# Kernel optimization log

Hardware: AMD Instinct MI355X
Metric: run time of the kernel (lower is better)

The kernel has to match this reference:

```python
import jax, jax.numpy as jnp
import numpy as np

N, D, E, OUT = 10000, 15, 320, 30
H_INOUT = 5  # n_heads for in/out attention layers


def mha(q, k, v, wqkv, bqkv, wo, bo, nheads):
    # q,k,v: [B, L, E]; torch.nn.MultiheadAttention math (unbatched per node)
    B, L, Ed = q.shape
    hd = Ed // nheads
    wq, wk, wv = jnp.split(wqkv, 3, axis=0)
    bq, bk, bv = jnp.split(bqkv, 3)
    q2 = (q @ wq.T + bq).reshape(B, L, nheads, hd)
    k2 = (k @ wk.T + bk).reshape(B, -1, nheads, hd)
    v2 = (v @ wv.T + bv).reshape(B, -1, nheads, hd)
    scores = jnp.einsum('blhd,bmhd->bhlm', q2, k2) * (hd ** -0.5)
    a = jax.nn.softmax(scores, axis=-1)
    o = jnp.einsum('bhlm,bmhd->blhd', a, v2).reshape(B, L, Ed)
    return o @ wo.T + bo


def attn_layer(seq, Wq, Wk, Wv, wqkv, bqkv, wo, bo, nheads):
    # AttentionLayer: custom Q/K/V projections then MultiheadAttention
    return mha(seq @ Wq, seq @ Wk, seq @ Wv, wqkv, bqkv, wo, bo, nheads)


def setup_inputs() -> dict:
    key = jax.random.key(0)
    ks = jax.random.split(key, 24)
    s = 0.05  # scale params small for numerically stable softmax
    inp = {
        'X': jax.random.normal(ks[0], (N, E), jnp.float32),
        'in_idx': jax.random.randint(ks[1], (N, D), 0, N),
        'out_idx': jax.random.randint(ks[2], (N, D), 0, N),
        'in_Wq': jax.random.uniform(ks[3], (E, E)) * s,
        'in_Wk': jax.random.uniform(ks[4], (E, E)) * s,
        'in_Wv': jax.random.uniform(ks[5], (E, E)) * s,
        'in_qkv_w': jax.random.normal(ks[6], (3 * E, E)) * s,
        'in_qkv_b': jax.random.normal(ks[7], (3 * E,)) * s,
        'in_o_w': jax.random.normal(ks[8], (E, E)) * s,
        'in_o_b': jax.random.normal(ks[9], (E,)) * s,
        'out_Wq': jax.random.uniform(ks[10], (E, E)) * s,
        'out_Wk': jax.random.uniform(ks[11], (E, E)) * s,
        'out_Wv': jax.random.uniform(ks[12], (E, E)) * s,
        'out_qkv_w': jax.random.normal(ks[13], (3 * E, E)) * s,
        'out_qkv_b': jax.random.normal(ks[14], (3 * E,)) * s,
        'out_o_w': jax.random.normal(ks[15], (E, E)) * s,
        'out_o_b': jax.random.normal(ks[16], (E,)) * s,
        'fin_qkv_w': jax.random.normal(ks[17], (3 * E, E)) * s,
        'fin_qkv_b': jax.random.normal(ks[18], (3 * E,)) * s,
        'fin_o_w': jax.random.normal(ks[19], (E, E)) * s,
        'fin_o_b': jax.random.normal(ks[20], (E,)) * s,
        'W': jax.random.uniform(ks[21], (E, OUT)) * s,
    }
    return inp


def reference(X, in_idx, out_idx, in_Wq, in_Wk, in_Wv, in_qkv_w, in_qkv_b,
              in_o_w, in_o_b, out_Wq, out_Wk, out_Wv, out_qkv_w, out_qkv_b,
              out_o_w, out_o_b, fin_qkv_w, fin_qkv_b, fin_o_w, fin_o_b, W):
    # per-node sequence: [self ; neighbors] -> [N, D+1, E]
    seq_in = jnp.concatenate([X[:, None, :], X[in_idx]], axis=1)
    seq_out = jnp.concatenate([X[:, None, :], X[out_idx]], axis=1)
    a_in = attn_layer(seq_in, in_Wq, in_Wk, in_Wv, in_qkv_w, in_qkv_b,
                      in_o_w, in_o_b, H_INOUT)
    a_out = attn_layer(seq_out, out_Wq, out_Wk, out_Wv, out_qkv_w, out_qkv_b,
                       out_o_w, out_o_b, H_INOUT)
    att = jnp.concatenate([a_in, a_out], axis=1)  # [N, 2(D+1), E]
    fin = mha(att, att, att, fin_qkv_w, fin_qkv_b, fin_o_w, fin_o_b, 1)
    # first token of final attention per node -> project -> ELU
    return jax.nn.elu(fin[:, 0, :] @ W)
```

## Files before the change

### kernel.cpp

```cpp
#include <hip/hip_runtime.h>
#include <hip/hip_bf16.h>

typedef __hip_bfloat16 bf16;
typedef __bf16 nbf;
typedef nbf bf16x8 __attribute__((ext_vector_type(8)));
typedef float f32x4 __attribute__((ext_vector_type(4)));

#define NNODE 10000
#define DDEG  15
#define EE    320
#define LL    16
#define NH    5
#define HD    64
#define OUTD  30
#define PCOLS 1920
#define KF    642
#define TST   644

__global__ void detect_dtype_kernel(const unsigned int* __restrict__ X, int* __restrict__ flag)
{
    __shared__ int cnt;
    if (threadIdx.x == 0) cnt = 0;
    __syncthreads();
    int local = 0;
    for (int i = threadIdx.x; i < 1024; i += 256) {
        unsigned int lo = X[i] & 0xFFFFu;
        int e = (int)((lo >> 7) & 0xFFu);
        if (e >= 100 && e <= 140) local++;
    }
    atomicAdd(&cnt, local);
    __syncthreads();
    if (threadIdx.x == 0) *flag = (cnt > 512) ? 1 : 0;
}

__global__ void convert_bf_kernel(const void* __restrict__ src, nbf* __restrict__ dst,
                                  int n, const int* __restrict__ flag)
{
    int i = blockIdx.x * 256 + threadIdx.x;
    if (i >= n) return;
    if (*flag) dst[i] = ((const nbf*)src)[i];
    else       dst[i] = (nbf)(((const float*)src)[i]);
}

#define NSEG 18
struct ConvTab {
    const void* src[NSEG];
    void*       dst[NSEG];
    int         n[NSEG];
    int         tobf[NSEG];
};

__global__ void convert_batch_kernel(ConvTab t, const int* __restrict__ flag)
{
    const int seg = blockIdx.y;
    const int i = blockIdx.x * 256 + threadIdx.x;
    if (i >= t.n[seg]) return;
    float v = (*flag) ? (float)(((const nbf*)t.src[seg])[i]) : ((const float*)t.src[seg])[i];
    if (t.tobf[seg]) ((nbf*)t.dst[seg])[i] = (nbf)v;
    else             ((float*)t.dst[seg])[i] = v;
}

__global__ __launch_bounds__(256) void transpose3_kernel(const void* s0, const void* s1,
        const void* s2, nbf* __restrict__ dstbase, const int* __restrict__ flag)
{
    const void* src = (blockIdx.z == 0) ? s0 : (blockIdx.z == 1) ? s1 : s2;
    nbf* dst = dstbase + (size_t)blockIdx.z * EE * EE;
    __shared__ nbf tile[32][33];
    const int bx = blockIdx.x * 32, by = blockIdx.y * 32;
    const int tx = threadIdx.x & 31, ty = threadIdx.x >> 5;
    const int f = *flag;
    #pragma unroll
    for (int i = 0; i < 4; ++i) {
        const int r = by + ty + i * 8;
        float v = f ? (float)(((const nbf*)src)[(long)r * EE + bx + tx])
                    : ((const float*)src)[(long)r * EE + bx + tx];
        tile[ty + i * 8][tx] = (nbf)v;
    }
    __syncthreads();
    #pragma unroll
    for (int i = 0; i < 4; ++i) {
        const int r = bx + ty + i * 8;
        dst[(long)r * EE + by + tx] = tile[tx][ty + i * 8];
    }
}

__device__ __forceinline__ void stor(float* p, float v) { *p = v; }
__device__ __forceinline__ void stor(bf16* p, float v) { *p = __float2bfloat16(v); }

template<bool AT, bool BT, typename OT>
__global__ __launch_bounds__(256) void gemm_k(const float* __restrict__ A, int lda,
                       const float* __restrict__ B, int ldb,
                       const float* __restrict__ bias,
                       OT* __restrict__ C, int ldc, int M, int Nn, int K)
{
    __shared__ float As[16][65];
    __shared__ float Bs[16][65];
    const int tid = threadIdx.x;
    const int tx = tid & 15, ty = tid >> 4;
    const int n0 = blockIdx.x * 64, m0 = blockIdx.y * 64;
    float acc[4][4] = {};
    for (int k0 = 0; k0 < K; k0 += 16) {
        if constexpr (AT) {
            for (int i = tid; i < 1024; i += 256) {
                int kk = i >> 6, r = i & 63;
                int gm = m0 + r, gk = k0 + kk;
                As[kk][r] = (gm < M && gk < K) ? A[(long)gk * lda + gm] : 0.f;
            }
        } else {
            for (int i = tid; i < 1024; i += 256) {
                int r = i >> 4, kk = i & 15;
                int gm = m0 + r, gk = k0 + kk;
                As[kk][r] = (gm < M && gk < K) ? A[(long)gm * lda + gk] : 0.f;
            }
        }
        if constexpr (BT) {
            for (int i = tid; i < 1024; i += 256) {
                int r = i >> 4, kk = i & 15;
                int gn = n0 + r, gk = k0 + kk;
                Bs[kk][r] = (gn < Nn && gk < K) ? B[(long)gn * ldb + gk] : 0.f;
            }
        } else {
            for (int i = tid; i < 1024; i += 256) {
                int kk = i >> 6, c = i & 63;
                int gk = k0 + kk, gn = n0 + c;
                Bs[kk][c] = (gk < K && gn < Nn) ? B[(long)gk * ldb + gn] : 0.f;
            }
        }
        __syncthreads();
        #pragma unroll
        for (int kk = 0; kk < 16; ++kk) {
            float ra[4], rb[4];
            #pragma unroll
            for (int a = 0; a < 4; ++a) ra[a] = As[kk][ty * 4 + a];
            #pragma unroll
            for (int b = 0; b < 4; ++b) rb[b] = Bs[kk][tx * 4 + b];
            #pragma unroll
            for (int a = 0; a < 4; ++a)
                #pragma unroll
                for (int b = 0; b < 4; ++b)
                    acc[a][b] += ra[a] * rb[b];
        }
        __syncthreads();
    }
    #pragma unroll
    for (int a = 0; a < 4; ++a) {
        int gm = m0 + ty * 4 + a;
        if (gm >= M) continue;
        #pragma unroll
        for (int b = 0; b < 4; ++b) {
            int gn = n0 + tx * 4 + b;
            if (gn >= Nn) continue;
            float v = acc[a][b] + (bias ? bias[gn] : 0.f);
            stor(&C[(long)gm * ldc + gn], v);
        }
    }
}

template<typename OT>
__global__ __launch_bounds__(256) void gemm_mfma(const nbf* __restrict__ A, int lda,
        const nbf* __restrict__ Bt, int ldb, const float* __restrict__ bias,
        OT* __restrict__ C, int ldc, int M, int Nn, int K)
{
    __shared__ __align__(16) nbf As[128][40];
    __shared__ __align__(16) nbf Bs[128][40];
    const int tid = threadIdx.x;
    const int lane = tid & 63, wave = tid >> 6;
    const int wr = (wave >> 1) * 64, wc = (wave & 1) * 64;
    const int m0 = blockIdx.y * 128, n0 = blockIdx.x * 128;
    const int lr = lane & 15, lq = lane >> 4;
    f32x4 acc[4][4];
    #pragma unroll
    for (int i = 0; i < 4; ++i)
        #pragma unroll
        for (int j = 0; j < 4; ++j) { acc[i][j][0]=0.f; acc[i][j][1]=0.f; acc[i][j][2]=0.f; acc[i][j][3]=0.f; }

    for (int k0 = 0; k0 < K; k0 += 32) {
        #pragma unroll
        for (int v = tid; v < 512; v += 256) {
            const int row = v >> 2, cv = (v & 3) << 3;
            const int gk = k0 + cv;
            {
                const int gm = m0 + row;
                bf16x8 val;
                if (gm < M && gk + 8 <= K) {
                    val = *(const bf16x8*)(A + (long)gm * lda + gk);
                } else {
                    union { bf16x8 v8; nbf e[8]; } u;
                    #pragma unroll
                    for (int j = 0; j < 8; ++j) {
                        float x = (gm < M && gk + j < K) ? (float)A[(long)gm * lda + gk + j] : 0.f;
                        u.e[j] = (nbf)x;
                    }
                    val = u.v8;
                }
                *(bf16x8*)&As[row][cv] = val;
            }
            {
                const int gn = n0 + row;
                bf16x8 val;
                if (gn < Nn && gk + 8 <= K) {
                    val = *(const bf16x8*)(Bt + (long)gn * ldb + gk);
                } else {
                    union { bf16x8 v8; nbf e[8]; } u;
                    #pragma unroll
                    for (int j = 0; j < 8; ++j) {
                        float x = (gn < Nn && gk + j < K) ? (float)Bt[(long)gn * ldb + gk + j] : 0.f;
                        u.e[j] = (nbf)x;
                    }
                    val = u.v8;
                }
                *(bf16x8*)&Bs[row][cv] = val;
            }
        }
        __syncthreads();
        bf16x8 af[4], bfv[4];
        #pragma unroll
        for (int i = 0; i < 4; ++i) af[i] = *(const bf16x8*)&As[wr + i * 16 + lr][lq * 8];
        #pragma unroll
        for (int j = 0; j < 4; ++j) bfv[j] = *(const bf16x8*)&Bs[wc + j * 16 + lr][lq * 8];
        #pragma unroll
        for (int i = 0; i < 4; ++i)
            #pragma unroll
            for (int j = 0; j < 4; ++j)
                acc[i][j] = __builtin_amdgcn_mfma_f32_16x16x32_bf16(af[i], bfv[j], acc[i][j], 0, 0, 0);
        __syncthreads();
    }
    #pragma unroll
    for (int i = 0; i < 4; ++i) {
        #pragma unroll
        for (int j = 0; j < 4; ++j) {
            const int gn = n0 + wc + j * 16 + lr;
            if (gn >= Nn) continue;
            const float bv = bias ? bias[gn] : 0.f;
            #pragma unroll
            for (int r = 0; r < 4; ++r) {
                const int gm = m0 + wr + i * 16 + lq * 4 + r;
                if (gm < M) stor(&C[(long)gm * ldc + gn], acc[i][j][r] + bv);
            }
        }
    }
}

#define NJOB 11
struct JobTab {
    const nbf* A[NJOB];
    const nbf* B[NJOB];
    nbf*       C[NJOB];
};

__global__ __launch_bounds__(256) void gemm_mfma_jobs(JobTab jt)
{
    const nbf* A  = jt.A[blockIdx.z];
    const nbf* Bt = jt.B[blockIdx.z];
    nbf* C        = jt.C[blockIdx.z];
    __shared__ __align__(16) nbf As[128][40];
    __shared__ __align__(16) nbf Bs[128][40];
    const int tid = threadIdx.x;
    const int lane = tid & 63, wave = tid >> 6;
    const int wr = (wave >> 1) * 64, wc = (wave & 1) * 64;
    const int m0 = blockIdx.y * 128, n0 = blockIdx.x * 128;
    const int lr = lane & 15, lq = lane >> 4;
    f32x4 acc[4][4];
    #pragma unroll
    for (int i = 0; i < 4; ++i)
        #pragma unroll
        for (int j = 0; j < 4; ++j) { acc[i][j][0]=0.f; acc[i][j][1]=0.f; acc[i][j][2]=0.f; acc[i][j][3]=0.f; }
    for (int k0 = 0; k0 < EE; k0 += 32) {
        #pragma unroll
        for (int v = tid; v < 512; v += 256) {
            const int row = v >> 2, cv = (v & 3) << 3;
            const int gk = k0 + cv;
            const int gm = m0 + row, gn = n0 + row;
            bf16x8 va = {}, vb = {};
            if (gm < EE) va = *(const bf16x8*)(A + (long)gm * EE + gk);
            if (gn < EE) vb = *(const bf16x8*)(Bt + (long)gn * EE + gk);
            *(bf16x8*)&As[row][cv] = va;
            *(bf16x8*)&Bs[row][cv] = vb;
        }
        __syncthreads();
        bf16x8 af[4], bfv[4];
        #pragma unroll
        for (int i = 0; i < 4; ++i) af[i] = *(const bf16x8*)&As[wr + i * 16 + lr][lq * 8];
        #pragma unroll
        for (int j = 0; j < 4; ++j) bfv[j] = *(const bf16x8*)&Bs[wc + j * 16 + lr][lq * 8];
        #pragma unroll
        for (int i = 0; i < 4; ++i)
            #pragma unroll
            for (int j = 0; j < 4; ++j)
                acc[i][j] = __builtin_amdgcn_mfma_f32_16x16x32_bf16(af[i], bfv[j], acc[i][j], 0, 0, 0);
        __syncthreads();
    }
    #pragma unroll
    for (int i = 0; i < 4; ++i)
        #pragma unroll
        for (int j = 0; j < 4; ++j) {
            const int gn = n0 + wc + j * 16 + lr;
            if (gn >= EE) continue;
            #pragma unroll
            for (int r = 0; r < 4; ++r) {
                const int gm = m0 + wr + i * 16 + lq * 4 + r;
                if (gm < EE) C[(long)gm * EE + gn] = (nbf)acc[i][j][r];
            }
        }
}

__global__ __launch_bounds__(320) void compose_bias_kernel(
        const float* __restrict__ in_o_b, const float* __restrict__ out_o_b,
        const float* __restrict__ fin_qkv_w, const float* __restrict__ fin_qkv_b,
        float* __restrict__ bqc_in, nbf* __restrict__ Kcat, nbf* __restrict__ VcatN)
{
    const int which = blockIdx.x;
    const int b = threadIdx.x;
    const float* ob = (which == 2 || which == 4) ? out_o_b : in_o_b;
    const int off = (which == 0) ? 0 : (which <= 2) ? 320 : 640;
    float acc = fin_qkv_b[off + b];
    const float* wr = fin_qkv_w + (long)(off + b) * EE;
    for (int e = 0; e < EE; ++e) acc += ob[e] * wr[e];
    if (which == 0)      bqc_in[b] = acc;
    else if (which == 1) Kcat[(long)640 * EE + b] = (nbf)acc;
    else if (which == 2) Kcat[(long)641 * EE + b] = (nbf)acc;
    else if (which == 3) VcatN[(long)640 * EE + b] = (nbf)acc;
    else                 VcatN[(long)641 * EE + b] = (nbf)acc;
}

__global__ void compose_bfin(const float* __restrict__ fin_o_b, const float* __restrict__ W,
                             float* __restrict__ bfin)
{
    int j = threadIdx.x;
    if (j >= OUTD) return;
    float acc = 0.f;
    for (int e = 0; e < EE; ++e) acc += fin_o_b[e] * W[e * OUTD + j];
    bfin[j] = acc;
}

__global__ void compose_bT(const float* __restrict__ bqc, const nbf* __restrict__ Kcat,
                           float* __restrict__ bT)
{
    int c = blockIdx.x * 256 + threadIdx.x;
    if (c >= KF) return;
    const nbf* kr = Kcat + (long)c * EE;
    float acc = 0.f;
    for (int b = 0; b < EE; ++b) acc += bqc[b] * (float)kr[b];
    bT[c] = acc;
}

__global__ void ut_prep_kernel(const float* __restrict__ WWT, nbf* __restrict__ Ut)
{
    int v = blockIdx.x * 256 + threadIdx.x;
    if (v >= 64 * EE) return;
    int n = v / EE, e = v % EE;
    float val = 0.f;
    if (n < OUTD) val = WWT[(long)n * KF + e];
    else if (n >= 32 && n < 32 + OUTD) val = WWT[(long)(n - 32) * KF + 320 + e];
    Ut[v] = (nbf)val;
}

__global__ __launch_bounds__(256) void row0_kernel(const nbf* __restrict__ P,
        const int* __restrict__ in_idx, nbf* __restrict__ Orow0)
{
    const int tid = threadIdx.x, lane = tid & 63, wave = tid >> 6;
    const int node = blockIdx.x * 4 + wave;
    __shared__ float a_sh[4][16];
    __shared__ int srcs_sh[4][16];
    const int m = lane & 15, q4 = lane >> 4;
    const int src = (m == 0) ? node : in_idx[node * DDEG + m - 1];
    if (q4 == 0) srcs_sh[wave][m] = src;
    const nbf* qrow = P + (long)node * PCOLS;
    const nbf* krow = P + (long)src * PCOLS + 320;
    #pragma unroll
    for (int h = 0; h < NH; ++h) {
        float s = 0.f;
        bf16x8 q1 = *(const bf16x8*)(qrow + h * 64 + q4 * 16);
        bf16x8 q2 = *(const bf16x8*)(qrow + h * 64 + q4 * 16 + 8);
        bf16x8 k1 = *(const bf16x8*)(krow + h * 64 + q4 * 16);
        bf16x8 k2 = *(const bf16x8*)(krow + h * 64 + q4 * 16 + 8);
        #pragma unroll
        for (int j = 0; j < 8; ++j)
            s += (float)q1[j] * (float)k1[j] + (float)q2[j] * (float)k2[j];
        s += __shfl_xor(s, 16);
        s += __shfl_xor(s, 32);
        s *= 0.125f;
        float mxv = s;
        #pragma unroll
        for (int msk = 8; msk >= 1; msk >>= 1) mxv = fmaxf(mxv, __shfl_xor(mxv, msk));
        float e = __expf(s - mxv);
        float es = e;
        #pragma unroll
        for (int msk = 8; msk >= 1; msk >>= 1) es += __shfl_xor(es, msk);
        if (q4 == 0) a_sh[wave][m] = e / es;
        float o = 0.f;
        #pragma unroll
        for (int mm = 0; mm < 16; ++mm)
            o += a_sh[wave][mm] * (float)P[(long)srcs_sh[wave][mm] * PCOLS + 640 + h * 64 + lane];
        Orow0[(long)node * EE + h * 64 + lane] = (nbf)o;
    }
}

__global__ __launch_bounds__(320) void mega_attn_kernel(const nbf* __restrict__ P,
        const int* __restrict__ in_idx, const int* __restrict__ out_idx,
        const float* __restrict__ T, const nbf* __restrict__ Ut,
        const float* __restrict__ WWT, const float* __restrict__ bfin,
        void* __restrict__ out, const int* __restrict__ flag)
{
    const int node = blockIdx.x;
    const int tid = threadIdx.x;
    const int lane = tid & 63, wave = tid >> 6;
    __shared__ __align__(16) nbf o_s[32][328];
    __shared__ __align__(16) nbf v_s[16][328];
    __shared__ __align__(16) nbf p_s[NH][16][16];
    __shared__ float s_red[2][16][8];
    __shared__ float s_fin[32];
    __shared__ float a_s[32];
    __shared__ float g_s[640];
    const int lr = lane & 15, lq = lane >> 4;
    const float* Trow = T + (long)node * TST;

    for (int d = 0; d < 2; ++d) {
        if (d) __syncthreads();
        const int* idx = d ? out_idx : in_idx;
        const long coloff = (long)d * 960;
        #pragma unroll
        for (int v = tid; v < 640; v += 320) {
            const int row = v / 40, c8 = (v % 40) * 8;
            const int src = (row == 0) ? node : idx[node * DDEG + row - 1];
            *(bf16x8*)&v_s[row][c8] = *(const bf16x8*)(P + (long)src * PCOLS + coloff + 640 + c8);
        }
        const int msrc = (lr == 0) ? node : idx[node * DDEG + lr - 1];
        const nbf* prow = P + (long)msrc * PCOLS + coloff;
        f32x4 sc = {0.f, 0.f, 0.f, 0.f};
        #pragma unroll
        for (int c = 0; c < 2; ++c) {
            bf16x8 aq = *(const bf16x8*)(prow + wave * 64 + c * 32 + lq * 8);
            bf16x8 bk = *(const bf16x8*)(prow + 320 + wave * 64 + c * 32 + lq * 8);
            sc = __builtin_amdgcn_mfma_f32_16x16x32_bf16(aq, bk, sc, 0, 0, 0);
        }
        float pr[4], mx4[4], sm4[4];
        #pragma unroll
        for (int r = 0; r < 4; ++r) { pr[r] = sc[r] * 0.125f; mx4[r] = pr[r]; }
        #pragma unroll
        for (int msk = 8; msk >= 1; msk >>= 1)
            #pragma unroll
            for (int r = 0; r < 4; ++r) mx4[r] = fmaxf(mx4[r], __shfl_xor(mx4[r], msk));
        #pragma unroll
        for (int r = 0; r < 4; ++r) { pr[r] = __expf(pr[r] - mx4[r]); sm4[r] = pr[r]; }
        #pragma unroll
        for (int msk = 8; msk >= 1; msk >>= 1)
            #pragma unroll
            for (int r = 0; r < 4; ++r) sm4[r] += __shfl_xor(sm4[r], msk);
        #pragma unroll
        for (int r = 0; r < 4; ++r) p_s[wave][lq * 4 + r][lr] = (nbf)(pr[r] / sm4[r]);
        union { bf16x8 v8; nbf e[8]; } pf;
        #pragma unroll
        for (int j = 0; j < 8; ++j) pf.e[j] = (nbf)0.f;
        if (lq < 2) pf.v8 = *(const bf16x8*)&p_s[wave][lr][lq * 8];
        __syncthreads();
        float spart = 0.f;
        #pragma unroll
        for (int t = 0; t < 4; ++t) {
            const int e0 = wave * 64 + t * 16;
            union { bf16x8 v8; nbf e[8]; } af;
            #pragma unroll
            for (int j = 0; j < 8; ++j) af.e[j] = (nbf)0.f;
            if (lq < 2) {
                #pragma unroll
                for (int j = 0; j < 8; ++j) af.e[j] = v_s[lq * 8 + j][e0 + lr];
            }
            f32x4 ov = {0.f, 0.f, 0.f, 0.f};
            ov = __builtin_amdgcn_mfma_f32_16x16x32_bf16(af.v8, pf.v8, ov, 0, 0, 0);
            union { unsigned long long u; nbf e[4]; } o4;
            #pragma unroll
            for (int r = 0; r < 4; ++r) o4.e[r] = (nbf)ov[r];
            *(unsigned long long*)&o_s[d * 16 + lr][e0 + lq * 4] = o4.u;
            f32x4 tv = *(const f32x4*)(Trow + d * 320 + e0 + lq * 4);
            spart += ov[0] * tv[0] + ov[1] * tv[1] + ov[2] * tv[2] + ov[3] * tv[3];
        }
        spart += __shfl_xor(spart, 16);
        spart += __shfl_xor(spart, 32);
        if (lq == 0) s_red[d][lr][wave] = spart;
    }
    __syncthreads();
    if (tid < 32) {
        const int d = tid >> 4, m = tid & 15;
        float s = 0.f;
        #pragma unroll
        for (int w = 0; w < NH; ++w) s += s_red[d][m][w];
        s += Trow[640 + d];
        s_fin[tid] = s * 0.05590169943749474f;
    }
    __syncthreads();
    float mx = -1e30f;
    #pragma unroll 4
    for (int m = 0; m < 32; ++m) mx = fmaxf(mx, s_fin[m]);
    float esum = 0.f, a_in = 0.f, a_out = 0.f;
    #pragma unroll 4
    for (int m = 0; m < 32; ++m) {
        float e = __expf(s_fin[m] - mx);
        esum += e;
        if (m < 16) a_in += e; else a_out += e;
    }
    const float inv = 1.f / esum;
    a_in *= inv; a_out *= inv;
    if (tid < 32) a_s[tid] = __expf(s_fin[tid] - mx) * inv;
    __syncthreads();
    #pragma unroll
    for (int v = tid; v < 640; v += 320) {
        const int mbase = (v < 320) ? 0 : 16;
        const int e = (v < 320) ? v : v - 320;
        float g = 0.f;
        #pragma unroll
        for (int m2 = 0; m2 < 16; ++m2)
            g += a_s[mbase + m2] * (float)o_s[mbase + m2][e];
        g_s[v] = g;
    }
    __syncthreads();
    const int j = tid >> 3, sub = tid & 7;
    if (j < OUTD) {
        const nbf* u_in  = Ut + (long)j * EE;
        const nbf* u_out = Ut + (long)(32 + j) * EE;
        float acc = 0.f;
        for (int c = sub; c < 40; c += 8) {
            bf16x8 uv = *(const bf16x8*)(u_in + c * 8);
            bf16x8 uo = *(const bf16x8*)(u_out + c * 8);
            #pragma unroll
            for (int jj = 0; jj < 8; ++jj) {
                acc += g_s[c * 8 + jj] * (float)uv[jj];
                acc += g_s[320 + c * 8 + jj] * (float)uo[jj];
            }
        }
        acc += __shfl_down(acc, 4, 8);
        acc += __shfl_down(acc, 2, 8);
        acc += __shfl_down(acc, 1, 8);
        if (sub == 0) {
            float r = acc + a_in * WWT[(long)j * KF + 640]
                    + a_out * WWT[(long)j * KF + 641] + bfin[j];
            r = r > 0.f ? r : expm1f(r);
            if (*flag) ((bf16*)out)[(long)node * OUTD + j] = __float2bfloat16(r);
            else       ((float*)out)[(long)node * OUTD + j] = r;
        }
    }
}

extern "C" void kernel_launch(void* const* d_in, const int* in_sizes, int n_in,
                              void* d_out, int out_size, void* d_ws, size_t ws_size,
                              hipStream_t stream)
{
    const int* in_idx  = (const int*)d_in[1];
    const int* out_idx = (const int*)d_in[2];

    char* p = (char*)d_ws;
    auto alloc = [&](size_t bytes) { char* r = p; p += (bytes + 255) & ~(size_t)255; return r; };
    const size_t EE2 = (size_t)EE * EE;
    int*   flag       = (int*)alloc(256);
    nbf*   X_bf       = (nbf*)alloc((size_t)NNODE * EE * 2);
    nbf*   qkvw6_bf   = (nbf*)alloc(6 * EE2 * 2);
    nbf*   Wg6_bf     = (nbf*)alloc(6 * EE2 * 2);
    nbf*   qkvw_fin_bf= (nbf*)alloc(3 * EE2 * 2);
    nbf*   owT        = (nbf*)alloc(3 * EE2 * 2);
    float* qkvw_fin_f = (float*)alloc(3 * EE2 * 4);
    float* qkvb_fin_f = (float*)alloc(3 * EE * 4);
    float* bcat       = (float*)alloc(PCOLS * 4);
    float* ob_in_f    = (float*)alloc(EE * 4);
    float* ob_out_f   = (float*)alloc(EE * 4);
    float* ob_fin_f   = (float*)alloc(EE * 4);
    float* W_f        = (float*)alloc((size_t)EE * OUTD * 4);
    float* ow_fin_f   = (float*)alloc(EE2 * 4);
    nbf*   AcatT  = (nbf*)alloc((size_t)PCOLS * EE * 2);
    nbf*   Qc_bf  = (nbf*)alloc(EE2 * 2);
    nbf*   Kcat   = (nbf*)alloc((size_t)KF * EE * 2);
    float* bqc_in = (float*)alloc(EE * 4);
    nbf*   M2T    = (nbf*)alloc((size_t)KF * EE * 2);
    float* bT     = (float*)alloc(KF * 4);
    nbf*   VcatN  = (nbf*)alloc((size_t)KF * EE * 2);
    nbf*   WfinT  = (nbf*)alloc((size_t)OUTD * EE * 2);
    float* WWT    = (float*)alloc((size_t)OUTD * KF * 4);
    float* bfin   = (float*)alloc(64 * 4);
    nbf*   Ut     = (nbf*)alloc((size_t)64 * EE * 2);
    nbf*   P      = (nbf*)alloc((size_t)NNODE * PCOLS * 2);
    nbf*   Orow0  = (nbf*)alloc((size_t)NNODE * EE * 2);
    float* Tm     = (float*)alloc((size_t)NNODE * TST * 4);

    dim3 blk(256);
    detect_dtype_kernel<<<1, blk, 0, stream>>>((const unsigned int*)d_in[0], flag);
    convert_bf_kernel<<<(NNODE * EE + 255) / 256, blk, 0, stream>>>(d_in[0], X_bf, NNODE * EE, flag);
    ConvTab ct;
    int s = 0;
    auto seg = [&](const void* src, void* dst, int n, int tobf) {
        ct.src[s] = src; ct.dst[s] = dst; ct.n[s] = n; ct.tobf[s] = tobf; ++s;
    };
    seg(d_in[6],  qkvw6_bf,           (int)(3 * EE2), 1);
    seg(d_in[13], qkvw6_bf + 3 * EE2, (int)(3 * EE2), 1);
    seg(d_in[3],  Wg6_bf + 0 * EE2, (int)EE2, 1);
    seg(d_in[4],  Wg6_bf + 1 * EE2, (int)EE2, 1);
    seg(d_in[5],  Wg6_bf + 2 * EE2, (int)EE2, 1);
    seg(d_in[10], Wg6_bf + 3 * EE2, (int)EE2, 1);
    seg(d_in[11], Wg6_bf + 4 * EE2, (int)EE2, 1);
    seg(d_in[12], Wg6_bf + 5 * EE2, (int)EE2, 1);
    seg(d_in[17], qkvw_fin_bf, (int)(3 * EE2), 1);
    seg(d_in[17], qkvw_fin_f,  (int)(3 * EE2), 0);
    seg(d_in[18], qkvb_fin_f, 3 * EE, 0);
    seg(d_in[7],  bcat,       3 * EE, 0);
    seg(d_in[14], bcat + 960, 3 * EE, 0);
    seg(d_in[9],  ob_in_f,  EE, 0);
    seg(d_in[16], ob_out_f, EE, 0);
    seg(d_in[20], ob_fin_f, EE, 0);
    seg(d_in[21], W_f, EE * OUTD, 0);
    seg(d_in[19], ow_fin_f, (int)EE2, 0);
    convert_batch_kernel<<<dim3((3 * (int)EE2 + 255) / 256, NSEG), blk, 0, stream>>>(ct, flag);
    transpose3_kernel<<<dim3(10, 10, 3), blk, 0, stream>>>(d_in[8], d_in[15], d_in[19], owT, flag);

    JobTab jt;
    for (int g = 0; g < 6; ++g) {
        jt.A[g] = qkvw6_bf + (size_t)g * EE2;
        jt.B[g] = Wg6_bf + (size_t)g * EE2;
        jt.C[g] = AcatT + (size_t)g * EE2;
    }
    jt.A[6] = owT;             jt.B[6] = qkvw_fin_bf;                      jt.C[6] = Qc_bf;
    jt.A[7] = owT;             jt.B[7] = qkvw_fin_bf + (size_t)320 * EE;   jt.C[7] = Kcat;
    jt.A[8] = owT + EE2;       jt.B[8] = qkvw_fin_bf + (size_t)320 * EE;   jt.C[8] = Kcat + (size_t)320 * EE;
    jt.A[9] = owT;             jt.B[9] = qkvw_fin_bf + (size_t)640 * EE;   jt.C[9] = VcatN;
    jt.A[10]= owT + EE2;       jt.B[10]= qkvw_fin_bf + (size_t)640 * EE;   jt.C[10]= VcatN + (size_t)320 * EE;
    gemm_mfma_jobs<<<dim3(3, 3, NJOB), blk, 0, stream>>>(jt);
    compose_bias_kernel<<<5, 320, 0, stream>>>(ob_in_f, ob_out_f, qkvw_fin_f, qkvb_fin_f,
                                               bqc_in, Kcat, VcatN);
    gemm_mfma<bf16><<<dim3(3, 6), blk, 0, stream>>>(
        Kcat, EE, Qc_bf, EE, nullptr, (bf16*)M2T, EE, KF, EE, EE);
    compose_bT<<<3, blk, 0, stream>>>(bqc_in, Kcat, bT);
    gemm_k<true, false, bf16><<<dim3(5, 1), blk, 0, stream>>>(
        W_f, OUTD, ow_fin_f, EE, nullptr, (bf16*)WfinT, EE, OUTD, EE, EE);
    gemm_mfma<float><<<dim3(6, 1), blk, 0, stream>>>(
        WfinT, EE, VcatN, EE, nullptr, WWT, KF, OUTD, KF, EE);
    compose_bfin<<<1, 64, 0, stream>>>(ob_fin_f, W_f, bfin);
    ut_prep_kernel<<<(64 * EE + 255) / 256, blk, 0, stream>>>(WWT, Ut);

    gemm_mfma<bf16><<<dim3(PCOLS / 128, (NNODE + 127) / 128), blk, 0, stream>>>(
        X_bf, EE, AcatT, EE, bcat, (bf16*)P, PCOLS, NNODE, PCOLS, EE);

    row0_kernel<<<NNODE / 4, blk, 0, stream>>>(P, in_idx, Orow0);

    gemm_mfma<float><<<dim3((KF + 127) / 128, (NNODE + 127) / 128), blk, 0, stream>>>(
        Orow0, EE, M2T, EE, bT, Tm, TST, NNODE, KF, EE);

    mega_attn_kernel<<<NNODE, dim3(320), 0, stream>>>(
        P, in_idx, out_idx, Tm, Ut, WWT, bfin, d_out, flag);
}
```

Before: 593.6 us.

## Split attention into per-direction Y projection kernel and per-node combine kernel

The per-node mega kernel is split so each block handles one direction (in or out). A block computes the attention output and projects it through Ut, plus the T row, with MFMA into a 16x32 Y tile, which is written to a chunked global buffer. A separate combine kernel then does the final softmax and weighted sum over the 32 Y rows per node. T is now stored in bf16 instead of fp32. This doubles the block count, removes the large o_s/g_s shared buffers and the scalar final GEMV, and turns the projection into matrix-core work. The cost is an extra global round trip for Y, an extra launch per chunk, and lower precision for T.

```diff
diff --git a/kernel.cpp b/kernel.cpp
--- a/kernel.cpp
+++ b/kernel.cpp
@@ -15,7 +15,7 @@
 #define OUTD  30
 #define PCOLS 1920
 #define KF    642
-#define TST   644
+#define TSTB  648
 
 __global__ void detect_dtype_kernel(const unsigned int* __restrict__ X, int* __restrict__ flag)
 {
@@ -396,147 +396,151 @@
     }
 }
 
-__global__ __launch_bounds__(320) void mega_attn_kernel(const nbf* __restrict__ P,
+__global__ __launch_bounds__(320) void attn_y_kernel(const nbf* __restrict__ P,
         const int* __restrict__ in_idx, const int* __restrict__ out_idx,
-        const float* __restrict__ T, const nbf* __restrict__ Ut,
-        const float* __restrict__ WWT, const float* __restrict__ bfin,
-        void* __restrict__ out, const int* __restrict__ flag)
-{
-    const int node = blockIdx.x;
+        const nbf* __restrict__ Tb, const nbf* __restrict__ Ut,
+        float* __restrict__ Ygl, int node_base)
+{
+    const int bx = blockIdx.x;
+    const int lnode = bx >> 1, d = bx & 1;
+    const int node = node_base + lnode;
     const int tid = threadIdx.x;
     const int lane = tid & 63, wave = tid >> 6;
-    __shared__ __align__(16) nbf o_s[32][328];
     __shared__ __align__(16) nbf v_s[16][328];
     __shared__ __align__(16) nbf p_s[NH][16][16];
-    __shared__ float s_red[2][16][8];
-    __shared__ float s_fin[32];
-    __shared__ float a_s[32];
-    __shared__ float g_s[640];
+    __shared__ float Yp[NH][16][32];
+    const int* idx = d ? out_idx : in_idx;
+    const long coloff = (long)d * 960;
     const int lr = lane & 15, lq = lane >> 4;
-    const float* Trow = T + (long)node * TST;
-
-    for (int d = 0; d < 2; ++d) {
-        if (d) __syncthreads();
-        const int* idx = d ? out_idx : in_idx;
-        const long coloff = (long)d * 960;
-        #pragma unroll
-        for (int v = tid; v < 640; v += 320) {
-            const int row = v / 40, c8 = (v % 40) * 8;
-            const int src = (row == 0) ? node : idx[node * DDEG + row - 1];
-            *(bf16x8*)&v_s[row][c8] = *(const bf16x8*)(P + (long)src * PCOLS + coloff + 640 + c8);
-        }
-        const int msrc = (lr == 0) ? node : idx[node * DDEG + lr - 1];
-        const nbf* prow = P + (long)msrc * PCOLS + coloff;
-        f32x4 sc = {0.f, 0.f, 0.f, 0.f};
-        #pragma unroll
-        for (int c = 0; c < 2; ++c) {
-            bf16x8 aq = *(const bf16x8*)(prow + wave * 64 + c * 32 + lq * 8);
-            bf16x8 bk = *(const bf16x8*)(prow + 320 + wave * 64 + c * 32 + lq * 8);
-            sc = __builtin_amdgcn_mfma_f32_16x16x32_bf16(aq, bk, sc, 0, 0, 0);
-        }
-        float pr[4], mx4[4], sm4[4];
-        #pragma unroll
-        for (int r = 0; r < 4; ++r) { pr[r] = sc[r] * 0.125f; mx4[r] = pr[r]; }
-        #pragma unroll
-        for (int msk = 8; msk >= 1; msk >>= 1)
-            #pragma unroll
-            for (int r = 0; r < 4; ++r) mx4[r] = fmaxf(mx4[r], __shfl_xor(mx4[r], msk));
-        #pragma unroll
-        for (int r = 0; r < 4; ++r) { pr[r] = __expf(pr[r] - mx4[r]); sm4[r] = pr[r]; }
-        #pragma unroll
-        for (int msk = 8; msk >= 1; msk >>= 1)
-            #pragma unroll
-            for (int r = 0; r < 4; ++r) sm4[r] += __shfl_xor(sm4[r], msk);
-        #pragma unroll
-        for (int r = 0; r < 4; ++r) p_s[wave][lq * 4 + r][lr] = (nbf)(pr[r] / sm4[r]);
-        union { bf16x8 v8; nbf e[8]; } pf;
-        #pragma unroll
-        for (int j = 0; j < 8; ++j) pf.e[j] = (nbf)0.f;
-        if (lq < 2) pf.v8 = *(const bf16x8*)&p_s[wave][lr][lq * 8];
-        __syncthreads();
-        float spart = 0.f;
-        #pragma unroll
-        for (int t = 0; t < 4; ++t) {
-            const int e0 = wave * 64 + t * 16;
-            union { bf16x8 v8; nbf e[8]; } af;
-            #pragma unroll
-            for (int j = 0; j < 8; ++j) af.e[j] = (nbf)0.f;
-            if (lq < 2) {
-                #pragma unroll
-                for (int j = 0; j < 8; ++j) af.e[j] = v_s[lq * 8 + j][e0 + lr];
-            }
-            f32x4 ov = {0.f, 0.f, 0.f, 0.f};
-            ov = __builtin_amdgcn_mfma_f32_16x16x32_bf16(af.v8, pf.v8, ov, 0, 0, 0);
-            union { unsigned long long u; nbf e[4]; } o4;
-            #pragma unroll
-            for (int r = 0; r < 4; ++r) o4.e[r] = (nbf)ov[r];
-            *(unsigned long long*)&o_s[d * 16 + lr][e0 + lq * 4] = o4.u;
-            f32x4 tv = *(const f32x4*)(Trow + d * 320 + e0 + lq * 4);
-            spart += ov[0] * tv[0] + ov[1] * tv[1] + ov[2] * tv[2] + ov[3] * tv[3];
-        }
-        spart += __shfl_xor(spart, 16);
-        spart += __shfl_xor(spart, 32);
-        if (lq == 0) s_red[d][lr][wave] = spart;
-    }
+    #pragma unroll
+    for (int v = tid; v < 640; v += 320) {
+        const int row = v / 40, c8 = (v % 40) * 8;
+        const int src = (row == 0) ? node : idx[node * DDEG + row - 1];
+        *(bf16x8*)&v_s[row][c8] = *(const bf16x8*)(P + (long)src * PCOLS + coloff + 640 + c8);
+    }
+    const int msrc = (lr == 0) ? node : idx[node * DDEG + lr - 1];
+    const nbf* prow = P + (long)msrc * PCOLS + coloff;
+    f32x4 sc = {0.f, 0.f, 0.f, 0.f};
+    #pragma unroll
+    for (int c = 0; c < 2; ++c) {
+        bf16x8 aq = *(const bf16x8*)(prow + wave * 64 + c * 32 + lq * 8);
+        bf16x8 bk = *(const bf16x8*)(prow + 320 + wave * 64 + c * 32 + lq * 8);
+        sc = __builtin_amdgcn_mfma_f32_16x16x32_bf16(aq, bk, sc, 0, 0, 0);
+    }
+    float pr[4], mx4[4], sm4[4];
+    #pragma unroll
+    for (int r = 0; r < 4; ++r) { pr[r] = sc[r] * 0.125f; mx4[r] = pr[r]; }
+    #pragma unroll
+    for (int msk = 8; msk >= 1; msk >>= 1)
+        #pragma unroll
+        for (int r = 0; r < 4; ++r) mx4[r] = fmaxf(mx4[r], __shfl_xor(mx4[r], msk));
+    #pragma unroll
+    for (int r = 0; r < 4; ++r) { pr[r] = __expf(pr[r] - mx4[r]); sm4[r] = pr[r]; }
+    #pragma unroll
+    for (int msk = 8; msk >= 1; msk >>= 1)
+        #pragma unroll
+        for (int r = 0; r < 4; ++r) sm4[r] += __shfl_xor(sm4[r], msk);
+    #pragma unroll
+    for (int r = 0; r < 4; ++r) p_s[wave][lq * 4 + r][lr] = (nbf)(pr[r] / sm4[r]);
+    union { bf16x8 v8; nbf e[8]; } pf;
+    #pragma unroll
+    for (int j = 0; j < 8; ++j) pf.e[j] = (nbf)0.f;
+    if (lq < 2) pf.v8 = *(const bf16x8*)&p_s[wave][lr][lq * 8];
     __syncthreads();
-    if (tid < 32) {
-        const int d = tid >> 4, m = tid & 15;
-        float s = 0.f;
-        #pragma unroll
-        for (int w = 0; w < NH; ++w) s += s_red[d][m][w];
-        s += Trow[640 + d];
-        s_fin[tid] = s * 0.05590169943749474f;
-    }
+    #pragma unroll
+    for (int t = 0; t < 4; ++t) {
+        const int e0 = wave * 64 + t * 16;
+        union { bf16x8 v8; nbf e[8]; } af;
+        #pragma unroll
+        for (int j = 0; j < 8; ++j) af.e[j] = (nbf)0.f;
+        if (lq < 2) {
+            #pragma unroll
+            for (int j = 0; j < 8; ++j) af.e[j] = v_s[lq * 8 + j][e0 + lr];
+        }
+        f32x4 ov = {0.f, 0.f, 0.f, 0.f};
+        ov = __builtin_amdgcn_mfma_f32_16x16x32_bf16(af.v8, pf.v8, ov, 0, 0, 0);
+        union { unsigned long long u; nbf e[4]; } o4;
+        #pragma unroll
+        for (int r = 0; r < 4; ++r) o4.e[r] = (nbf)ov[r];
+        *(unsigned long long*)&v_s[lr][e0 + lq * 4] = o4.u;
+    }
+    const nbf* Utd = Ut + (long)d * 32 * EE;
+    const nbf* TbRow = Tb + (long)node * TSTB + (long)d * 320;
+    f32x4 yacc[2];
+    yacc[0][0]=0.f; yacc[0][1]=0.f; yacc[0][2]=0.f; yacc[0][3]=0.f;
+    yacc[1][0]=0.f; yacc[1][1]=0.f; yacc[1][2]=0.f; yacc[1][3]=0.f;
+    const int e0w = wave * 64;
+    #pragma unroll
+    for (int c = 0; c < 2; ++c) {
+        const int kk = e0w + c * 32 + lq * 8;
+        bf16x8 afy = *(const bf16x8*)&v_s[lr][kk];
+        #pragma unroll
+        for (int nt = 0; nt < 2; ++nt) {
+            const int row = nt * 16 + lr;
+            const nbf* bp = (row == 31) ? (TbRow + kk) : (Utd + (long)row * EE + kk);
+            bf16x8 bfy = *(const bf16x8*)bp;
+            yacc[nt] = __builtin_amdgcn_mfma_f32_16x16x32_bf16(afy, bfy, yacc[nt], 0, 0, 0);
+        }
+    }
+    #pragma unroll
+    for (int nt = 0; nt < 2; ++nt)
+        #pragma unroll
+        for (int r = 0; r < 4; ++r)
+            Yp[wave][lq * 4 + r][nt * 16 + lr] = yacc[nt][r];
     __syncthreads();
+    float* yout = Ygl + (long)(lnode * 2 + d) * 512;
+    for (int v = tid; v < 512; v += 320) {
+        float sme = 0.f;
+        #pragma unroll
+        for (int w = 0; w < NH; ++w) sme += Yp[w][v >> 5][v & 31];
+        yout[v] = sme;
+    }
+}
+
+__global__ __launch_bounds__(256) void combine_kernel(const float* __restrict__ Ygl,
+        const nbf* __restrict__ Tb, const float* __restrict__ WWT,
+        const float* __restrict__ bfin, void* __restrict__ out,
+        long obase, int cnt, const int* __restrict__ flag)
+{
+    const int tid = threadIdx.x, lane = tid & 63, wave = tid >> 6;
+    const int node = blockIdx.x * 4 + wave;
+    const int nodec = (node < cnt) ? node : (cnt - 1);
+    __shared__ float Yl[4][1024];
+    __shared__ float sf[4][32];
+    const float* ysrc = Ygl + (long)nodec * 1024;
+    #pragma unroll
+    for (int v = lane; v < 1024; v += 64) Yl[wave][v] = ysrc[v];
+    if (lane < 32) {
+        const int d = lane >> 4, m = lane & 15;
+        sf[wave][lane] = (Yl[wave][d * 512 + m * 32 + 31]
+                          + (float)Tb[(long)nodec * TSTB + 640 + d]) * 0.05590169943749474f;
+    }
     float mx = -1e30f;
     #pragma unroll 4
-    for (int m = 0; m < 32; ++m) mx = fmaxf(mx, s_fin[m]);
+    for (int m = 0; m < 32; ++m) mx = fmaxf(mx, sf[wave][m]);
     float esum = 0.f, a_in = 0.f, a_out = 0.f;
     #pragma unroll 4
     for (int m = 0; m < 32; ++m) {
-        float e = __expf(s_fin[m] - mx);
+        float e = __expf(sf[wave][m] - mx);
         esum += e;
         if (m < 16) a_in += e; else a_out += e;
     }
     const float inv = 1.f / esum;
     a_in *= inv; a_out *= inv;
-    if (tid < 32) a_s[tid] = __expf(s_fin[tid] - mx) * inv;
-    __syncthreads();
-    #pragma unroll
-    for (int v = tid; v < 640; v += 320) {
-        const int mbase = (v < 320) ? 0 : 16;
-        const int e = (v < 320) ? v : v - 320;
-        float g = 0.f;
-        #pragma unroll
-        for (int m2 = 0; m2 < 16; ++m2)
-            g += a_s[mbase + m2] * (float)o_s[mbase + m2][e];
-        g_s[v] = g;
-    }
-    __syncthreads();
-    const int j = tid >> 3, sub = tid & 7;
-    if (j < OUTD) {
-        const nbf* u_in  = Ut + (long)j * EE;
-        const nbf* u_out = Ut + (long)(32 + j) * EE;
+    const int j = lane;
+    if (j < OUTD && node < cnt) {
         float acc = 0.f;
-        for (int c = sub; c < 40; c += 8) {
-            bf16x8 uv = *(const bf16x8*)(u_in + c * 8);
-            bf16x8 uo = *(const bf16x8*)(u_out + c * 8);
-            #pragma unroll
-            for (int jj = 0; jj < 8; ++jj) {
-                acc += g_s[c * 8 + jj] * (float)uv[jj];
-                acc += g_s[320 + c * 8 + jj] * (float)uo[jj];
-            }
-        }
-        acc += __shfl_down(acc, 4, 8);
-        acc += __shfl_down(acc, 2, 8);
-        acc += __shfl_down(acc, 1, 8);
-        if (sub == 0) {
-            float r = acc + a_in * WWT[(long)j * KF + 640]
-                    + a_out * WWT[(long)j * KF + 641] + bfin[j];
-            r = r > 0.f ? r : expm1f(r);
-            if (*flag) ((bf16*)out)[(long)node * OUTD + j] = __float2bfloat16(r);
-            else       ((float*)out)[(long)node * OUTD + j] = r;
-        }
+        #pragma unroll 4
+        for (int dm = 0; dm < 32; ++dm) {
+            const int d = dm >> 4, m = dm & 15;
+            float a = __expf(sf[wave][dm] - mx) * inv;
+            acc += a * Yl[wave][d * 512 + m * 32 + j];
+        }
+        float r = acc + a_in * WWT[(long)j * KF + 640]
+                + a_out * WWT[(long)j * KF + 641] + bfin[j];
+        r = r > 0.f ? r : expm1f(r);
+        if (*flag) ((bf16*)out)[obase + (long)node * OUTD + j] = __float2bfloat16(r);
+        else       ((float*)out)[obase + (long)node * OUTD + j] = r;
     }
 }
 
@@ -577,7 +581,15 @@
     nbf*   Ut     = (nbf*)alloc((size_t)64 * EE * 2);
     nbf*   P      = (nbf*)alloc((size_t)NNODE * PCOLS * 2);
     nbf*   Orow0  = (nbf*)alloc((size_t)NNODE * EE * 2);
-    float* Tm     = (float*)alloc((size_t)NNODE * TST * 4);
+    nbf*   Tb     = (nbf*)alloc((size_t)NNODE * TSTB * 2);
+    size_t fixed = (size_t)(p - (char*)d_ws);
+
+    const size_t per_node = 1024 * 4;
+    size_t avail = (ws_size > fixed + 65536) ? (ws_size - fixed - 65536) : 0;
+    long chunk_l = (long)(avail / per_node);
+    chunk_l = (chunk_l / 4) * 4;
+    int chunk = (chunk_l > NNODE) ? NNODE : (chunk_l < 4 ? 4 : (int)chunk_l);
+    float* Ygl = (float*)alloc((size_t)chunk * 1024 * 4);
 
     dim3 blk(256);
     detect_dtype_kernel<<<1, blk, 0, stream>>>((const unsigned int*)d_in[0], flag);
@@ -637,9 +649,14 @@
 
     row0_kernel<<<NNODE / 4, blk, 0, stream>>>(P, in_idx, Orow0);
 
-    gemm_mfma<float><<<dim3((KF + 127) / 128, (NNODE + 127) / 128), blk, 0, stream>>>(
-        Orow0, EE, M2T, EE, bT, Tm, TST, NNODE, KF, EE);
-
-    mega_attn_kernel<<<NNODE, dim3(320), 0, stream>>>(
-        P, in_idx, out_idx, Tm, Ut, WWT, bfin, d_out, flag);
-}
+    gemm_mfma<bf16><<<dim3((KF + 127) / 128, (NNODE + 127) / 128), blk, 0, stream>>>(
+        Orow0, EE, M2T, EE, bT, (bf16*)Tb, TSTB, NNODE, KF, EE);
+
+    for (int base = 0; base < NNODE; base += chunk) {
+        int cnt = (NNODE - base < chunk) ? (NNODE - base) : chunk;
+        attn_y_kernel<<<2 * cnt, dim3(320), 0, stream>>>(
+            P, in_idx, out_idx, Tb, Ut, Ygl, base);
+        combine_kernel<<<(cnt + 3) / 4, blk, 0, stream>>>(
+            Ygl, Tb + (size_t)base * TSTB, WWT, bfin, d_out, (long)base * OUTD, cnt, flag);
+    }
+}
```

Result: faster. 497.1 us (-16.3%).
